# Kernel tuning notes

Hardware: AMD Instinct MI355X
Metric: run time of the kernel (lower is better)

Reference implementation:

```python
import jax, jax.numpy as jnp
import numpy as np

TAU = 2.0          # LIF membrane time constant (tau=2.0 in module)
SG_ALPHA = 4.0     # spikingjelly default Sigmoid surrogate alpha


def lif(x, v_th=1.0):
    """MultiStepLIFNode: leaky-integrate-fire over leading time dim T.
    v <- v + (x - v)/tau ; spike = H(v - v_th) ; hard reset v <- 0 where spiked.
    Surrogate gradient (sigmoid) via straight-through for backward.
    x: [T, ...] -> spikes: [T, ...]
    """
    def step(v, xt):
        v = v + (xt - v) / TAU
        sg = jax.nn.sigmoid(SG_ALPHA * (v - v_th))
        hard = (v >= v_th).astype(xt.dtype)
        spike = jax.lax.stop_gradient(hard - sg) + sg
        # detach_reset=True: reset path does not carry gradient
        v = v * (1.0 - jax.lax.stop_gradient(spike))
        return v, spike
    v0 = jnp.zeros_like(x[0])
    _, s = jax.lax.scan(step, v0, x)
    return s


def bn_c(x, scale, bias):
    """Inference-mode BatchNorm folded to per-channel affine; x: [T,B,C,N]."""
    return x * scale[None, None, :, None] + bias[None, None, :, None]


def setup_inputs() -> dict:
    T, B, C, H, W = 4, 32, 512, 14, 14
    Ch = int(C * 4.0)  # mlp hidden
    key = jax.random.key(0)
    ks = jax.random.split(key, 16)
    std = 0.05
    d = {
        'x': jax.random.normal(ks[0], (T, B, C, H, W), jnp.float32),
        'q_w': jax.random.normal(ks[1], (C, C), jnp.float32) * std,
        'q_bn_s': 1.0 + 0.1 * jax.random.normal(ks[2], (C,), jnp.float32),
        'q_bn_b': 0.1 * jax.random.normal(ks[3], (C,), jnp.float32),
        'k_w': jax.random.normal(ks[4], (C, C), jnp.float32) * std,
        'k_bn_s': 1.0 + 0.1 * jax.random.normal(ks[5], (C,), jnp.float32),
        'k_bn_b': 0.1 * jax.random.normal(ks[6], (C,), jnp.float32),
        'proj_w': jax.random.normal(ks[7], (C, C), jnp.float32) * std,
        'proj_b': 0.1 * jax.random.normal(ks[8], (C,), jnp.float32),
        'proj_bn_s': 1.0 + 0.1 * jax.random.normal(ks[9], (C,), jnp.float32),
        'proj_bn_b': 0.1 * jax.random.normal(ks[10], (C,), jnp.float32),
        'mlp1_w': jax.random.normal(ks[11], (Ch, C), jnp.float32) * std,
        'mlp1_b': 0.1 * jax.random.normal(ks[12], (Ch,), jnp.float32),
        'mlp1_bn_s': 1.0 + 0.1 * jax.random.normal(ks[13], (Ch,), jnp.float32),
        'mlp1_bn_b': 0.1 * jax.random.normal(ks[14], (Ch,), jnp.float32),
        'mlp2_w': jax.random.normal(ks[15], (C, Ch), jnp.float32) * std,
        'mlp2_b': 0.1 * jax.random.normal(jax.random.fold_in(key, 100), (C,), jnp.float32),
        'mlp2_bn_s': 1.0 + 0.1 * jax.random.normal(jax.random.fold_in(key, 101), (C,), jnp.float32),
        'mlp2_bn_b': 0.1 * jax.random.normal(jax.random.fold_in(key, 102), (C,), jnp.float32),
    }
    return d


NUM_HEADS = 8


def reference(x, q_w, q_bn_s, q_bn_b, k_w, k_bn_s, k_bn_b,
              proj_w, proj_b, proj_bn_s, proj_bn_b,
              mlp1_w, mlp1_b, mlp1_bn_s, mlp1_bn_b,
              mlp2_w, mlp2_b, mlp2_bn_s, mlp2_bn_b):
    T, B, C, H, W = x.shape
    N = H * W
    h = NUM_HEADS
    Chd = C // h
    xf = x.reshape(T, B, C, N)

    # ---- Token_QK_Attention ----
    q_sp = lif(bn_c(jnp.einsum('oc,tbcn->tbon', q_w, xf), q_bn_s, q_bn_b))
    k_sp = lif(bn_c(jnp.einsum('oc,tbcn->tbon', k_w, xf), k_bn_s, k_bn_b))
    # per-head channel sum of q spikes: [T,B,h,1,N]
    q_sum = q_sp.reshape(T, B, h, Chd, N).sum(axis=3, keepdims=True)
    attn_sp = lif(q_sum, v_th=0.5)                       # attn_lif, v_threshold=0.5
    x_one = attn_sp * k_sp.reshape(T, B, h, Chd, N)      # spiking multiply
    x_one = x_one.reshape(T, B, C, N)
    p = jnp.einsum('oc,tbcn->tbon', proj_w, x_one) + proj_b[None, None, :, None]
    y = lif(bn_c(p, proj_bn_s, proj_bn_b)).reshape(T, B, C, H, W)
    x = x + y                                            # residual

    # ---- MLP ----
    xf = x.reshape(T, B, C, N)
    h1 = jnp.einsum('oc,tbcn->tbon', mlp1_w, xf) + mlp1_b[None, None, :, None]
    h1 = lif(bn_c(h1, mlp1_bn_s, mlp1_bn_b))
    h2 = jnp.einsum('oc,tbcn->tbon', mlp2_w, h1) + mlp2_b[None, None, :, None]
    h2 = lif(bn_c(h2, mlp2_bn_s, mlp2_bn_b))
    return x + h2.reshape(T, B, C, H, W)
```

## Files before the change

kernel.cpp:

```cpp
#include <hip/hip_runtime.h>
#include <cstdint>

#define NT  4
#define NB  32
#define NC  512
#define NCH 2048
#define NN  196
#define NM  (NB * NN)
#define NH  8

struct GP {
    const float *q_bn_s, *q_bn_b, *k_bn_s, *k_bn_b;
    const float *proj_b, *proj_bn_s, *proj_bn_b;
    const float *mlp1_b, *mlp1_bn_s, *mlp1_bn_b;
    const float *mlp2_b, *mlp2_bn_s, *mlp2_bn_b;
    const float *wqkT, *wprojT, *wmlp1T, *wmlp2T;
    const float *xT;
    float *xy;
    float *v_q, *v_k, *v_y, *v_h1, *v_h2, *v_attn;
    unsigned char *q_sp, *k_sp, *x_one, *h1_sp, *attn_sp;
    float *out;
    int t;
};

__device__ __forceinline__ float lif_step(float z, float v_old, float vth, int& sp) {
    float d = __fsub_rn(z, v_old);
    float h = __fmul_rn(d, 0.5f);
    float v = __fadd_rn(v_old, h);
    sp = (v >= vth) ? 1 : 0;
    return sp ? 0.0f : v;
}

typedef const void __attribute__((address_space(1))) gas_t;
typedef void __attribute__((address_space(3))) las_t;
__device__ __forceinline__ void gl_lds16(const float* g, float* l) {
    __builtin_amdgcn_global_load_lds((gas_t*)g, (las_t*)l, 16, 0, 0);
}
__device__ __forceinline__ void vm0() {
    asm volatile("s_waitcnt vmcnt(0)" ::: "memory");
}
__device__ __forceinline__ void vm3() {
    asm volatile("s_waitcnt vmcnt(3)" ::: "memory");
}
__device__ __forceinline__ void lgkm0() {
    asm volatile("s_waitcnt lgkmcnt(0)" ::: "memory");
}


__global__ __launch_bounds__(256) void trw_k(const float* __restrict__ src,
                                             float* __restrict__ dst,
                                             int K, int ldD, int offD) {
    __shared__ float tle[32][33];
    const int c0 = blockIdx.x * 32, o0 = blockIdx.y * 32;
    const int tx = threadIdx.x & 31, ty = threadIdx.x >> 5;
#pragma unroll
    for (int r = 0; r < 4; ++r)
        tle[ty + r * 8][tx] = src[(size_t)(o0 + ty + r * 8) * K + c0 + tx];
    __syncthreads();
#pragma unroll
    for (int r = 0; r < 4; ++r)
        dst[(size_t)(c0 + ty + r * 8) * ldD + offD + o0 + tx] = tle[tx][ty + r * 8];
}

__global__ __launch_bounds__(64) void permx_k(const float* __restrict__ x,
                                              float* __restrict__ xT) {
    const int id = blockIdx.x;
    const int b = id & 31;
    const int c = (id >> 5) & 511;
    const int t = id >> 14;
    const float* s = x + ((size_t)(t * NB + b) * NC + c) * NN;
    float* d = xT + ((size_t)(t * NC + c) * NB + b) * NN;
    for (int n = threadIdx.x; n < NN; n += 64) d[n] = s[n];
}

__global__ __launch_bounds__(256) void attn_k(GP gp) {
    const int m = blockIdx.x * 256 + threadIdx.x;
    const int h = blockIdx.y;
    if (m >= NM) return;
    const unsigned char* q = gp.q_sp + (size_t)h * 64 * NM + m;
    int s = 0;
#pragma unroll 8
    for (int d = 0; d < 64; ++d) s += q[(size_t)d * NM];
    float v = gp.t ? gp.v_attn[(size_t)h * NM + m] : 0.0f;
    int sp;
    v = lif_step((float)s, v, 0.5f, sp);
    gp.v_attn[(size_t)h * NM + m] = v;
    gp.attn_sp[(size_t)h * NM + m] = (unsigned char)sp;
}

__global__ __launch_bounds__(256) void xone_k(GP gp) {
    const int c = blockIdx.y;
    const int m4 = (blockIdx.x * 256 + threadIdx.x) * 4;
    if (m4 >= NM) return;
    const unsigned int kv = *(const unsigned int*)(gp.k_sp + (size_t)c * NM + m4);
    const unsigned int av = *(const unsigned int*)(gp.attn_sp + (size_t)(c >> 6) * NM + m4);
    *(unsigned int*)(gp.x_one + (size_t)c * NM + m4) = kv & av;
}

template <int MODE>
__global__ __launch_bounds__(64) void gemm_lif(GP gp) {
    constexpr bool FUSED = (MODE == 1 || MODE == 3);
    constexpr int K_TOT = (MODE == 3) ? 2048 : 512;
    constexpr int LDA = (MODE == 0) ? 1024 : (MODE == 2) ? 2048 : 512;
    constexpr int BK = 16;
    constexpr int NIT = K_TOT / BK;
    constexpr int MT = FUSED ? 32 : 64;
    constexpr int RN = FUSED ? 4 : 8;
    constexpr int NBUF = FUSED ? 4 : 2;
    constexpr int XP = FUSED ? 36 : MT;

    __shared__ float As[NBUF][BK][32];
    __shared__ float Xs[NBUF][BK][XP];

    const int lane = threadIdx.x;
    const int to = lane & 7;
    const int tn = lane >> 3;
    const int m0 = blockIdx.x * MT;
    const int ot = blockIdx.y;
    const int o0 = ot * 32;
    const int mb = m0 + tn * RN;

    const float* wA = (MODE == 0) ? gp.wqkT : (MODE == 1) ? gp.wprojT
                    : (MODE == 2) ? gp.wmlp1T : gp.wmlp2T;
    const float* xf = (MODE == 0) ? gp.xT + (size_t)gp.t * NC * NM : gp.xy;
    const unsigned char* xu = (MODE == 1) ? gp.x_one : gp.h1_sp;

    auto stageA = [&](int buf, int s) {
#pragma unroll
        for (int r = 0; r < 2; ++r)
            gl_lds16(wA + (size_t)(s * BK + r * 8 + (lane >> 3)) * LDA + o0 + (lane & 7) * 4,
                     &As[buf][r * 8][0]);
    };
    auto stageXf = [&](int buf, int s) {
#pragma unroll
        for (int r = 0; r < 4; ++r)
            gl_lds16(xf + (size_t)(s * BK + r * 4 + (lane >> 4)) * NM + m0 + (lane & 15) * 4,
                     &Xs[buf][r * 4][0]);
    };
    const int xrow = lane >> 2;
    const int xcb = (lane & 3) * 8;
    auto loadB = [&](int s) -> uint2 {
        return *(const uint2*)(xu + (size_t)(s * BK + xrow) * NM + m0 + xcb);
    };
    auto flushB = [&](int buf, uint2 xb) {
        float* d = &Xs[buf][xrow][xcb];
        float4 f0, f1;
        f0.x = (float)(unsigned char)(xb.x);
        f0.y = (float)(unsigned char)(xb.x >> 8);
        f0.z = (float)(unsigned char)(xb.x >> 16);
        f0.w = (float)(xb.x >> 24);
        f1.x = (float)(unsigned char)(xb.y);
        f1.y = (float)(unsigned char)(xb.y >> 8);
        f1.z = (float)(unsigned char)(xb.y >> 16);
        f1.w = (float)(xb.y >> 24);
        *(float4*)d = f0;
        *(float4*)(d + 4) = f1;
    };

    float acc[4][RN];
#pragma unroll
    for (int i = 0; i < 4; ++i)
#pragma unroll
        for (int j = 0; j < RN; ++j) acc[i][j] = 0.0f;

    auto compute = [&](int cur) {
        if constexpr (!FUSED) {
#pragma unroll 4
            for (int kk = 0; kk < BK; ++kk) {
                const float4 av = *(const float4*)&As[cur][kk][to * 4];
                const float4 x0 = *(const float4*)&Xs[cur][kk][tn * 8];
                const float4 x1 = *(const float4*)&Xs[cur][kk][tn * 8 + 4];
                const float a4[4] = {av.x, av.y, av.z, av.w};
                const float x8[8] = {x0.x, x0.y, x0.z, x0.w, x1.x, x1.y, x1.z, x1.w};
#pragma unroll
                for (int i = 0; i < 4; ++i)
#pragma unroll
                    for (int j = 0; j < 8; ++j)
                        acc[i][j] = __fadd_rn(acc[i][j], __fmul_rn(a4[i], x8[j]));
            }
        } else {
#pragma unroll 8
            for (int kk = 0; kk < BK; ++kk) {
                const float4 av = *(const float4*)&As[cur][kk][to * 4];
                const float4 xv = *(const float4*)&Xs[cur][kk][tn * 4];
                const float a4[4] = {av.x, av.y, av.z, av.w};
                const float x4[4] = {xv.x, xv.y, xv.z, xv.w};
#pragma unroll
                for (int i = 0; i < 4; ++i)
#pragma unroll
                    for (int j = 0; j < 4; ++j)
                        acc[i][j] = __fmaf_rn(a4[i], x4[j], acc[i][j]);
            }
        }
    };

    if constexpr (!FUSED) {
        stageA(0, 0); stageXf(0, 0);
        vm0();
#pragma unroll 1
        for (int it = 0; it < NIT; ++it) {
            const int cur = it & 1;
            const bool more = (it + 1 < NIT);
            if (more) { stageA(cur ^ 1, it + 1); stageXf(cur ^ 1, it + 1); }
            compute(cur);
            if (more) vm0();
        }
    } else {
        uint2 sl0, sl1;
        stageA(0, 0); sl0 = loadB(0);
        stageA(1, 1); sl1 = loadB(1);
        vm3();
        flushB(0, sl0);
        lgkm0();

        auto body = [&](int i, int cb, uint2& sStage, uint2& sFlush) {
            if (i + 2 < NIT) { stageA((cb + 2) & 3, i + 2); sStage = loadB(i + 2); }
            compute(cb);
            if (i + 1 < NIT) {
                if (NIT - 1 - i >= 2) vm3(); else vm0();
                flushB((cb + 1) & 3, sFlush);
                lgkm0();
            }
        };
#pragma unroll 1
        for (int i = 0; i < NIT; i += 4) {
            body(i + 0, 0, sl0, sl1);
            body(i + 1, 1, sl1, sl0);
            body(i + 2, 2, sl0, sl1);
            body(i + 3, 3, sl1, sl0);
        }
    }

    if constexpr (MODE == 0) {
        const bool isq = (ot < 16);
        const float* bs = isq ? gp.q_bn_s : gp.k_bn_s;
        const float* bbv = isq ? gp.q_bn_b : gp.k_bn_b;
        float* vb = isq ? gp.v_q : gp.v_k;
        unsigned char* sb = isq ? gp.q_sp : gp.k_sp;
        const int ob = (ot & 15) * 32;
#pragma unroll
        for (int i = 0; i < 4; ++i) {
            const int oo = ob + to * 4 + i;
            const float sc = bs[oo], bc = bbv[oo];
            float* vr = vb + (size_t)oo * NM + mb;
            float vv[8];
            if (gp.t) {
                const float4 v0 = *(const float4*)vr, v1 = *(const float4*)(vr + 4);
                vv[0] = v0.x; vv[1] = v0.y; vv[2] = v0.z; vv[3] = v0.w;
                vv[4] = v1.x; vv[5] = v1.y; vv[6] = v1.z; vv[7] = v1.w;
            } else {
#pragma unroll
                for (int j = 0; j < 8; ++j) vv[j] = 0.0f;
            }
            unsigned int pk[2] = {0, 0};
#pragma unroll
            for (int j = 0; j < 8; ++j) {
                const float z = __fadd_rn(__fmul_rn(acc[i][j], sc), bc);
                int sp;
                vv[j] = lif_step(z, vv[j], 1.0f, sp);
                pk[j >> 2] |= (unsigned)sp << ((j & 3) * 8);
            }
            *(float4*)vr = make_float4(vv[0], vv[1], vv[2], vv[3]);
            *(float4*)(vr + 4) = make_float4(vv[4], vv[5], vv[6], vv[7]);
            *(unsigned int*)(sb + (size_t)oo * NM + mb) = pk[0];
            *(unsigned int*)(sb + (size_t)oo * NM + mb + 4) = pk[1];
        }
    } else if constexpr (MODE == 2) {
        const int ob = ot * 32;
#pragma unroll
        for (int i = 0; i < 4; ++i) {
            const int o = ob + to * 4 + i;
            const float bi = gp.mlp1_b[o], sc = gp.mlp1_bn_s[o], bc = gp.mlp1_bn_b[o];
            float* vr = gp.v_h1 + (size_t)o * NM + mb;
            float vv[8];
            if (gp.t) {
                const float4 v0 = *(const float4*)vr, v1 = *(const float4*)(vr + 4);
                vv[0] = v0.x; vv[1] = v0.y; vv[2] = v0.z; vv[3] = v0.w;
                vv[4] = v1.x; vv[5] = v1.y; vv[6] = v1.z; vv[7] = v1.w;
            } else {
#pragma unroll
                for (int j = 0; j < 8; ++j) vv[j] = 0.0f;
            }
            unsigned int pk[2] = {0, 0};
#pragma unroll
            for (int j = 0; j < 8; ++j) {
                const float z = __fadd_rn(__fmul_rn(__fadd_rn(acc[i][j], bi), sc), bc);
                int sp;
                vv[j] = lif_step(z, vv[j], 1.0f, sp);
                pk[j >> 2] |= (unsigned)sp << ((j & 3) * 8);
            }
            *(float4*)vr = make_float4(vv[0], vv[1], vv[2], vv[3]);
            *(float4*)(vr + 4) = make_float4(vv[4], vv[5], vv[6], vv[7]);
            *(unsigned int*)(gp.h1_sp + (size_t)o * NM + mb) = pk[0];
            *(unsigned int*)(gp.h1_sp + (size_t)o * NM + mb + 4) = pk[1];
        }
    } else if constexpr (MODE == 1) {
        const int ob = ot * 32;
#pragma unroll
        for (int i = 0; i < 4; ++i) {
            const int o = ob + to * 4 + i;
            const float bi = gp.proj_b[o], sc = gp.proj_bn_s[o], bc = gp.proj_bn_b[o];
            float* vr = gp.v_y + (size_t)o * NM + mb;
            const float4 vld = gp.t ? *(const float4*)vr : make_float4(0, 0, 0, 0);
            const float4 xv4 = *(const float4*)(gp.xT + ((size_t)gp.t * NC + o) * NM + mb);
            float vv[4] = {vld.x, vld.y, vld.z, vld.w};
            const float xvv[4] = {xv4.x, xv4.y, xv4.z, xv4.w};
            float xyo[4];
#pragma unroll
            for (int j = 0; j < 4; ++j) {
                const float z = __fadd_rn(__fmul_rn(__fadd_rn(acc[i][j], bi), sc), bc);
                int sp;
                vv[j] = lif_step(z, vv[j], 1.0f, sp);
                xyo[j] = __fadd_rn(xvv[j], (float)sp);
            }
            *(float4*)vr = make_float4(vv[0], vv[1], vv[2], vv[3]);
            *(float4*)(gp.xy + (size_t)o * NM + mb) = make_float4(xyo[0], xyo[1], xyo[2], xyo[3]);
        }
    } else {
        const int ob = ot * 32;
        const int b = mb / NN;
        const int n = mb - b * NN;
#pragma unroll
        for (int i = 0; i < 4; ++i) {
            const int o = ob + to * 4 + i;
            const float bi = gp.mlp2_b[o], sc = gp.mlp2_bn_s[o], bc = gp.mlp2_bn_b[o];
            float* vr = gp.v_h2 + (size_t)o * NM + mb;
            const float4 vld = gp.t ? *(const float4*)vr : make_float4(0, 0, 0, 0);
            const float4 xyv = *(const float4*)(gp.xy + (size_t)o * NM + mb);
            float vv[4] = {vld.x, vld.y, vld.z, vld.w};
            const float xyf[4] = {xyv.x, xyv.y, xyv.z, xyv.w};
            float ov[4];
#pragma unroll
            for (int j = 0; j < 4; ++j) {
                const float z = __fadd_rn(__fmul_rn(__fadd_rn(acc[i][j], bi), sc), bc);
                int sp;
                vv[j] = lif_step(z, vv[j], 1.0f, sp);
                ov[j] = __fadd_rn(xyf[j], (float)sp);
            }
            *(float4*)&gp.out[(((size_t)gp.t * NB + b) * NC + o) * NN + n] =
                make_float4(ov[0], ov[1], ov[2], ov[3]);
            *(float4*)vr = make_float4(vv[0], vv[1], vv[2], vv[3]);
        }
    }
}

extern "C" void kernel_launch(void* const* d_in, const int* in_sizes, int n_in,
                              void* d_out, int out_size, void* d_ws, size_t ws_size,
                              hipStream_t stream) {
    const float* x       = (const float*)d_in[0];
    const float* q_w     = (const float*)d_in[1];
    const float* k_w     = (const float*)d_in[4];
    const float* proj_w  = (const float*)d_in[7];
    const float* mlp1_w  = (const float*)d_in[11];
    const float* mlp2_w  = (const float*)d_in[15];

    GP gp;
    gp.q_bn_s = (const float*)d_in[2];  gp.q_bn_b = (const float*)d_in[3];
    gp.k_bn_s = (const float*)d_in[5];  gp.k_bn_b = (const float*)d_in[6];
    gp.proj_b = (const float*)d_in[8];  gp.proj_bn_s = (const float*)d_in[9];  gp.proj_bn_b = (const float*)d_in[10];
    gp.mlp1_b = (const float*)d_in[12]; gp.mlp1_bn_s = (const float*)d_in[13]; gp.mlp1_bn_b = (const float*)d_in[14];
    gp.mlp2_b = (const float*)d_in[16]; gp.mlp2_bn_s = (const float*)d_in[17]; gp.mlp2_bn_b = (const float*)d_in[18];
    gp.out = (float*)d_out;

    char* ws = (char*)d_ws;
    size_t off = 0;
    auto alloc = [&](size_t bytes) -> void* {
        void* r = ws + off;
        off += (bytes + 255) & ~(size_t)255;
        return r;
    };
    float* wqkT   = (float*)alloc((size_t)512 * 1024 * 4);
    float* wprojT = (float*)alloc((size_t)512 * 512 * 4);
    float* wmlp1T = (float*)alloc((size_t)512 * 2048 * 4);
    float* wmlp2T = (float*)alloc((size_t)2048 * 512 * 4);
    float* xT     = (float*)alloc((size_t)NT * NC * NM * 4);
    gp.xy     = (float*)alloc((size_t)NC * NM * 4);
    gp.v_q    = (float*)alloc((size_t)NC * NM * 4);
    gp.v_k    = (float*)alloc((size_t)NC * NM * 4);
    gp.v_y    = (float*)alloc((size_t)NC * NM * 4);
    gp.v_h2   = (float*)alloc((size_t)NC * NM * 4);
    gp.v_h1   = (float*)alloc((size_t)NCH * NM * 4);
    gp.v_attn = (float*)alloc((size_t)NH * NM * 4);
    gp.q_sp   = (unsigned char*)alloc((size_t)NC * NM);
    gp.k_sp   = (unsigned char*)alloc((size_t)NC * NM);
    gp.x_one  = (unsigned char*)alloc((size_t)NC * NM);
    gp.h1_sp  = (unsigned char*)alloc((size_t)NCH * NM);
    gp.attn_sp= (unsigned char*)alloc((size_t)NH * NM);
    gp.wqkT = wqkT; gp.wprojT = wprojT; gp.wmlp1T = wmlp1T; gp.wmlp2T = wmlp2T;
    gp.xT = xT;

    trw_k<<<dim3(16, 16), 256, 0, stream>>>(q_w,    wqkT,   512,  1024, 0);
    trw_k<<<dim3(16, 16), 256, 0, stream>>>(k_w,    wqkT,   512,  1024, 512);
    trw_k<<<dim3(16, 16), 256, 0, stream>>>(proj_w, wprojT, 512,  512,  0);
    trw_k<<<dim3(16, 64), 256, 0, stream>>>(mlp1_w, wmlp1T, 512,  2048, 0);
    trw_k<<<dim3(64, 16), 256, 0, stream>>>(mlp2_w, wmlp2T, 2048, 512,  0);
    permx_k<<<NT * NC * NB, 64, 0, stream>>>(x, xT);

    for (int t = 0; t < NT; ++t) {
        gp.t = t;
        gemm_lif<0><<<dim3(98, 32), 64, 0, stream>>>(gp);
        attn_k<<<dim3(25, NH), 256, 0, stream>>>(gp);
        xone_k<<<dim3(7, NC), 256, 0, stream>>>(gp);
        gemm_lif<1><<<dim3(196, 16), 64, 0, stream>>>(gp);
        gemm_lif<2><<<dim3(98, 64), 64, 0, stream>>>(gp);
        gemm_lif<3><<<dim3(196, 16), 64, 0, stream>>>(gp);
    }
}
```

Measured before the change: 2.517 ms.

## Bit-pack spike tensors and fuse spike multiply into projection GEMM load

Spike outputs (q, k, h1, attn) are stored as one bit per element instead of one byte, cutting the memory traffic of writing and reading spike matrices by a factor of eight. The separate x_one kernel is removed: the projection GEMM loads packed k and attn bits and ANDs them while staging into LDS, and the vmcnt wait is adjusted for the extra load. attn_k now counts bits per packed byte. The byte-wide loads become narrower and less coalesced, and the stores become single-byte writes.

```diff
diff --git a/kernel.cpp b/kernel.cpp
--- a/kernel.cpp
+++ b/kernel.cpp
@@ -7,6 +7,7 @@
 #define NCH 2048
 #define NN  196
 #define NM  (NB * NN)
+#define NMB (NM / 8)
 #define NH  8
 
 struct GP {
@@ -18,7 +19,7 @@
     const float *xT;
     float *xy;
     float *v_q, *v_k, *v_y, *v_h1, *v_h2, *v_attn;
-    unsigned char *q_sp, *k_sp, *x_one, *h1_sp, *attn_sp;
+    unsigned char *q_bt, *k_bt, *h1_bt, *attn_bt;
     float *out;
     int t;
 };
@@ -36,11 +37,14 @@
 __device__ __forceinline__ void gl_lds16(const float* g, float* l) {
     __builtin_amdgcn_global_load_lds((gas_t*)g, (las_t*)l, 16, 0, 0);
 }
+template <int N>
+__device__ __forceinline__ void vmwait() {
+    if constexpr (N == 0)      asm volatile("s_waitcnt vmcnt(0)" ::: "memory");
+    else if constexpr (N == 3) asm volatile("s_waitcnt vmcnt(3)" ::: "memory");
+    else if constexpr (N == 4) asm volatile("s_waitcnt vmcnt(4)" ::: "memory");
+}
 __device__ __forceinline__ void vm0() {
     asm volatile("s_waitcnt vmcnt(0)" ::: "memory");
-}
-__device__ __forceinline__ void vm3() {
-    asm volatile("s_waitcnt vmcnt(3)" ::: "memory");
 }
 __device__ __forceinline__ void lgkm0() {
     asm volatile("s_waitcnt lgkmcnt(0)" ::: "memory");
@@ -74,27 +78,31 @@
 }
 
 __global__ __launch_bounds__(256) void attn_k(GP gp) {
-    const int m = blockIdx.x * 256 + threadIdx.x;
-    const int h = blockIdx.y;
-    if (m >= NM) return;
-    const unsigned char* q = gp.q_sp + (size_t)h * 64 * NM + m;
-    int s = 0;
+    const int id = blockIdx.x * 256 + threadIdx.x;
+    if (id >= NH * NMB) return;
+    const int mB = id % NMB;
+    const int h = id / NMB;
+    int s[8];
+#pragma unroll
+    for (int j = 0; j < 8; ++j) s[j] = 0;
+    const unsigned char* q = gp.q_bt + (size_t)(h * 64) * NMB + mB;
 #pragma unroll 8
-    for (int d = 0; d < 64; ++d) s += q[(size_t)d * NM];
-    float v = gp.t ? gp.v_attn[(size_t)h * NM + m] : 0.0f;
-    int sp;
-    v = lif_step((float)s, v, 0.5f, sp);
-    gp.v_attn[(size_t)h * NM + m] = v;
-    gp.attn_sp[(size_t)h * NM + m] = (unsigned char)sp;
-}
-
-__global__ __launch_bounds__(256) void xone_k(GP gp) {
-    const int c = blockIdx.y;
-    const int m4 = (blockIdx.x * 256 + threadIdx.x) * 4;
-    if (m4 >= NM) return;
-    const unsigned int kv = *(const unsigned int*)(gp.k_sp + (size_t)c * NM + m4);
-    const unsigned int av = *(const unsigned int*)(gp.attn_sp + (size_t)(c >> 6) * NM + m4);
-    *(unsigned int*)(gp.x_one + (size_t)c * NM + m4) = kv & av;
+    for (int d = 0; d < 64; ++d) {
+        const unsigned b = q[(size_t)d * NMB];
+#pragma unroll
+        for (int j = 0; j < 8; ++j) s[j] += (b >> j) & 1;
+    }
+    unsigned ob = 0;
+#pragma unroll
+    for (int j = 0; j < 8; ++j) {
+        const int m = mB * 8 + j;
+        float v = gp.t ? gp.v_attn[(size_t)h * NM + m] : 0.0f;
+        int sp;
+        v = lif_step((float)s[j], v, 0.5f, sp);
+        gp.v_attn[(size_t)h * NM + m] = v;
+        ob |= (unsigned)sp << j;
+    }
+    gp.attn_bt[(size_t)h * NMB + mB] = (unsigned char)ob;
 }
 
 template <int MODE>
@@ -108,6 +116,7 @@
     constexpr int RN = FUSED ? 4 : 8;
     constexpr int NBUF = FUSED ? 4 : 2;
     constexpr int XP = FUSED ? 36 : MT;
+    constexpr int STW = (MODE == 1) ? 4 : 3;
 
     __shared__ float As[NBUF][BK][32];
     __shared__ float Xs[NBUF][BK][XP];
@@ -123,7 +132,6 @@
     const float* wA = (MODE == 0) ? gp.wqkT : (MODE == 1) ? gp.wprojT
                     : (MODE == 2) ? gp.wmlp1T : gp.wmlp2T;
     const float* xf = (MODE == 0) ? gp.xT + (size_t)gp.t * NC * NM : gp.xy;
-    const unsigned char* xu = (MODE == 1) ? gp.x_one : gp.h1_sp;
 
     auto stageA = [&](int buf, int s) {
 #pragma unroll
@@ -138,21 +146,32 @@
                      &Xs[buf][r * 4][0]);
     };
     const int xrow = lane >> 2;
-    const int xcb = (lane & 3) * 8;
+    const int xby = lane & 3;
+    const int mB8 = (m0 >> 3) + xby;
     auto loadB = [&](int s) -> uint2 {
-        return *(const uint2*)(xu + (size_t)(s * BK + xrow) * NM + m0 + xcb);
+        const int c = s * BK + xrow;
+        uint2 r;
+        if constexpr (MODE == 1) {
+            r.x = gp.k_bt[(size_t)c * NMB + mB8];
+            r.y = gp.attn_bt[(size_t)(c >> 6) * NMB + mB8];
+        } else {
+            r.x = gp.h1_bt[(size_t)c * NMB + mB8];
+            r.y = 0;
+        }
+        return r;
     };
     auto flushB = [&](int buf, uint2 xb) {
-        float* d = &Xs[buf][xrow][xcb];
+        const unsigned w = (MODE == 1) ? (xb.x & xb.y) : xb.x;
+        float* d = &Xs[buf][xrow][xby * 8];
         float4 f0, f1;
-        f0.x = (float)(unsigned char)(xb.x);
-        f0.y = (float)(unsigned char)(xb.x >> 8);
-        f0.z = (float)(unsigned char)(xb.x >> 16);
-        f0.w = (float)(xb.x >> 24);
-        f1.x = (float)(unsigned char)(xb.y);
-        f1.y = (float)(unsigned char)(xb.y >> 8);
-        f1.z = (float)(unsigned char)(xb.y >> 16);
-        f1.w = (float)(xb.y >> 24);
+        f0.x = (float)((w) & 1);
+        f0.y = (float)((w >> 1) & 1);
+        f0.z = (float)((w >> 2) & 1);
+        f0.w = (float)((w >> 3) & 1);
+        f1.x = (float)((w >> 4) & 1);
+        f1.y = (float)((w >> 5) & 1);
+        f1.z = (float)((w >> 6) & 1);
+        f1.w = (float)((w >> 7) & 1);
         *(float4*)d = f0;
         *(float4*)(d + 4) = f1;
     };
@@ -209,7 +228,7 @@
         uint2 sl0, sl1;
         stageA(0, 0); sl0 = loadB(0);
         stageA(1, 1); sl1 = loadB(1);
-        vm3();
+        vmwait<STW>();
         flushB(0, sl0);
         lgkm0();
 
@@ -217,7 +236,7 @@
             if (i + 2 < NIT) { stageA((cb + 2) & 3, i + 2); sStage = loadB(i + 2); }
             compute(cb);
             if (i + 1 < NIT) {
-                if (NIT - 1 - i >= 2) vm3(); else vm0();
+                if (NIT - 1 - i >= 2) vmwait<STW>(); else vmwait<0>();
                 flushB((cb + 1) & 3, sFlush);
                 lgkm0();
             }
@@ -236,8 +255,9 @@
         const float* bs = isq ? gp.q_bn_s : gp.k_bn_s;
         const float* bbv = isq ? gp.q_bn_b : gp.k_bn_b;
         float* vb = isq ? gp.v_q : gp.v_k;
-        unsigned char* sb = isq ? gp.q_sp : gp.k_sp;
+        unsigned char* sb = isq ? gp.q_bt : gp.k_bt;
         const int ob = (ot & 15) * 32;
+        const int mbB = (m0 >> 3) + tn;
 #pragma unroll
         for (int i = 0; i < 4; ++i) {
             const int oo = ob + to * 4 + i;
@@ -252,21 +272,21 @@
 #pragma unroll
                 for (int j = 0; j < 8; ++j) vv[j] = 0.0f;
             }
-            unsigned int pk[2] = {0, 0};
+            unsigned pb = 0;
 #pragma unroll
             for (int j = 0; j < 8; ++j) {
                 const float z = __fadd_rn(__fmul_rn(acc[i][j], sc), bc);
                 int sp;
                 vv[j] = lif_step(z, vv[j], 1.0f, sp);
-                pk[j >> 2] |= (unsigned)sp << ((j & 3) * 8);
+                pb |= (unsigned)sp << j;
             }
             *(float4*)vr = make_float4(vv[0], vv[1], vv[2], vv[3]);
             *(float4*)(vr + 4) = make_float4(vv[4], vv[5], vv[6], vv[7]);
-            *(unsigned int*)(sb + (size_t)oo * NM + mb) = pk[0];
-            *(unsigned int*)(sb + (size_t)oo * NM + mb + 4) = pk[1];
+            sb[(size_t)oo * NMB + mbB] = (unsigned char)pb;
         }
     } else if constexpr (MODE == 2) {
         const int ob = ot * 32;
+        const int mbB = (m0 >> 3) + tn;
 #pragma unroll
         for (int i = 0; i < 4; ++i) {
             const int o = ob + to * 4 + i;
@@ -281,18 +301,17 @@
 #pragma unroll
                 for (int j = 0; j < 8; ++j) vv[j] = 0.0f;
             }
-            unsigned int pk[2] = {0, 0};
+            unsigned pb = 0;
 #pragma unroll
             for (int j = 0; j < 8; ++j) {
                 const float z = __fadd_rn(__fmul_rn(__fadd_rn(acc[i][j], bi), sc), bc);
                 int sp;
                 vv[j] = lif_step(z, vv[j], 1.0f, sp);
-                pk[j >> 2] |= (unsigned)sp << ((j & 3) * 8);
+                pb |= (unsigned)sp << j;
             }
             *(float4*)vr = make_float4(vv[0], vv[1], vv[2], vv[3]);
             *(float4*)(vr + 4) = make_float4(vv[4], vv[5], vv[6], vv[7]);
-            *(unsigned int*)(gp.h1_sp + (size_t)o * NM + mb) = pk[0];
-            *(unsigned int*)(gp.h1_sp + (size_t)o * NM + mb + 4) = pk[1];
+            gp.h1_bt[(size_t)o * NMB + mbB] = (unsigned char)pb;
         }
     } else if constexpr (MODE == 1) {
         const int ob = ot * 32;
@@ -381,11 +400,10 @@
     gp.v_h2   = (float*)alloc((size_t)NC * NM * 4);
     gp.v_h1   = (float*)alloc((size_t)NCH * NM * 4);
     gp.v_attn = (float*)alloc((size_t)NH * NM * 4);
-    gp.q_sp   = (unsigned char*)alloc((size_t)NC * NM);
-    gp.k_sp   = (unsigned char*)alloc((size_t)NC * NM);
-    gp.x_one  = (unsigned char*)alloc((size_t)NC * NM);
-    gp.h1_sp  = (unsigned char*)alloc((size_t)NCH * NM);
-    gp.attn_sp= (unsigned char*)alloc((size_t)NH * NM);
+    gp.q_bt   = (unsigned char*)alloc((size_t)NC * NMB);
+    gp.k_bt   = (unsigned char*)alloc((size_t)NC * NMB);
+    gp.h1_bt  = (unsigned char*)alloc((size_t)NCH * NMB);
+    gp.attn_bt= (unsigned char*)alloc((size_t)NH * NMB);
     gp.wqkT = wqkT; gp.wprojT = wprojT; gp.wmlp1T = wmlp1T; gp.wmlp2T = wmlp2T;
     gp.xT = xT;
 
@@ -399,8 +417,7 @@
     for (int t = 0; t < NT; ++t) {
         gp.t = t;
         gemm_lif<0><<<dim3(98, 32), 64, 0, stream>>>(gp);
-        attn_k<<<dim3(25, NH), 256, 0, stream>>>(gp);
-        xone_k<<<dim3(7, NC), 256, 0, stream>>>(gp);
+        attn_k<<<dim3(25), 256, 0, stream>>>(gp);
         gemm_lif<1><<<dim3(196, 16), 64, 0, stream>>>(gp);
         gemm_lif<2><<<dim3(98, 64), 64, 0, stream>>>(gp);
         gemm_lif<3><<<dim3(196, 16), 64, 0, stream>>>(gp);
```

New measurement: 2.552 ms. About the same (+1.4%).
